# Optimization experiments

Hardware: AMD Instinct MI355X
Metric: run time of the kernel (lower is better)

The kernel has to match this reference:

```python
import jax, jax.numpy as jnp
import numpy as np

B, CIN, CMID, H, W = 2, 64, 128, 96, 96
KWIN = 7          # attention_window
DIL = 1           # attention_stride (dilation)
GROUPS = 16
EPS = 1e-5
SCALE = float(np.sqrt(CMID))  # torch: math.sqrt(intermediate_channels), multiplies logits (NATTEN semantics)


def group_norm(x, w, b):
    # x: [B,C,H,W], 16 groups, per-channel affine
    Bx, C, Hx, Wx = x.shape
    xg = x.reshape(Bx, GROUPS, C // GROUPS, Hx, Wx)
    mu = xg.mean(axis=(2, 3, 4), keepdims=True)
    var = xg.var(axis=(2, 3, 4), keepdims=True)
    xg = (xg - mu) * jax.lax.rsqrt(var + EPS)
    return xg.reshape(Bx, C, Hx, Wx) * w[None, :, None, None] + b[None, :, None, None]


def neighborhood_attention_2d(q, k, v, ksz, scale):
    # q,k,v: [B,H,W,C]; NATTEN-style neighborhood attention, dilation=1.
    Hh, Ww = q.shape[1], q.shape[2]
    half = ksz // 2
    # window start per query, clipped so every query sees exactly ksz keys per axis
    si = jnp.clip(jnp.arange(Hh) - half, 0, Hh - ksz)          # [H]
    sj = jnp.clip(jnp.arange(Ww) - half, 0, Ww - ksz)          # [W]
    idx_i = si[:, None] + jnp.arange(ksz)[None, :]             # [H,k]
    idx_j = sj[:, None] + jnp.arange(ksz)[None, :]             # [W,k]
    kw = k[:, idx_i][:, :, :, idx_j]                           # [B,H,k,W,k,C]
    vw = v[:, idx_i][:, :, :, idx_j]                           # [B,H,k,W,k,C]
    logits = jnp.einsum('bijc,biajkc->bijak', q, kw) * scale   # [B,H,W,k,k]
    Bq = logits.shape[0]
    attn = jax.nn.softmax(logits.reshape(Bq, Hh, Ww, ksz * ksz), axis=-1)
    attn = attn.reshape(Bq, Hh, Ww, ksz, ksz)
    return jnp.einsum('bijak,biajkc->bijc', attn, vw)          # [B,H,W,C]


def setup_inputs() -> dict:
    key = jax.random.key(0)
    ks = jax.random.split(key, 6)

    def wtz(k, shape, fan):
        return (jax.random.normal(k, shape, jnp.float32) / np.sqrt(fan)).astype(jnp.float32)

    return {
        'x': jax.random.normal(ks[0], (B, CIN, H, W), jnp.float32),
        'gn_w': jnp.ones((CIN,), jnp.float32),
        'gn_b': jnp.zeros((CIN,), jnp.float32),
        'conv_w': wtz(ks[1], (CMID, CIN, 3, 3), CIN * 9),
        'conv_b': jnp.zeros((CMID,), jnp.float32),
        'q_w': wtz(ks[2], (CMID, CMID), CMID),
        'q_b': jnp.zeros((CMID,), jnp.float32),
        'k_w': wtz(ks[3], (CMID, CMID), CMID),
        'k_b': jnp.zeros((CMID,), jnp.float32),
        'v_w': wtz(ks[4], (CMID, CMID), CMID),
        'v_b': jnp.zeros((CMID,), jnp.float32),
    }


def reference(x, gn_w, gn_b, conv_w, conv_b, q_w, q_b, k_w, k_b, v_w, v_b):
    xn = group_norm(x, gn_w, gn_b)
    # 3x3 conv, padding=1 + exact GELU (torch nn.GELU default)
    f = jax.lax.conv_general_dilated(
        xn, conv_w, window_strides=(1, 1), padding=((1, 1), (1, 1)),
        dimension_numbers=('NCHW', 'OIHW', 'NCHW')) + conv_b[None, :, None, None]
    f = jax.nn.gelu(f, approximate=False)
    # 1x1 QKV convs
    q = jnp.einsum('bchw,oc->bohw', f, q_w) + q_b[None, :, None, None]
    k = jnp.einsum('bchw,oc->bohw', f, k_w) + k_b[None, :, None, None]
    v = jnp.einsum('bchw,oc->bohw', f, v_w) + v_b[None, :, None, None]
    # to NHWC (singleton head dim squeezed)
    qh = q.transpose(0, 2, 3, 1)
    kh = k.transpose(0, 2, 3, 1)
    vh = v.transpose(0, 2, 3, 1)
    ksz = min(KWIN, f.shape[2], f.shape[3])
    ksz -= 1 if ksz % 2 == 0 else 0
    out = neighborhood_attention_2d(qh, kh, vh, ksz, SCALE)
    return out.transpose(0, 3, 1, 2)  # back to NCHW
```

## Files before the change

kernel.cpp:

```cpp
#include <hip/hip_runtime.h>
#include <math.h>

#define Hh 96
#define Ww 96
#define HW 9216
#define CIN 64
#define CMID 128
#define NAT_SCALE 11.313708498984761f

typedef __attribute__((ext_vector_type(4))) float f32x4;
typedef __attribute__((ext_vector_type(8))) short short8;

__device__ __forceinline__ unsigned short f2bf(float x) {
    union { float f; unsigned u; } v; v.f = x;
    unsigned r = v.u + 0x7FFF + ((v.u >> 16) & 1);
    return (unsigned short)(r >> 16);
}
__device__ __forceinline__ float bf2f(unsigned short h) {
    union { unsigned u; float f; } v; v.u = (unsigned)h << 16;
    return v.f;
}

__global__ __launch_bounds__(256) void prep_kernel(const float* __restrict__ x,
    float2* __restrict__ partials,
    const float* __restrict__ cw, const float* __restrict__ qw,
    const float* __restrict__ kw_, const float* __restrict__ vw,
    unsigned short* __restrict__ wch, unsigned short* __restrict__ wcl,
    unsigned short* __restrict__ wqh, unsigned short* __restrict__ wql)
{
    int bid = blockIdx.x, tid = threadIdx.x;
    if (bid < 512) {
        size_t base = (size_t)(bid >> 4) * 36864 + (size_t)(bid & 15) * 2304;
        float s = 0.f, s2 = 0.f;
        #pragma unroll
        for (int i = 0; i < 9; ++i) {
            float v = x[base + i * 256 + tid];
            s += v; s2 += v * v;
        }
        #pragma unroll
        for (int d = 1; d < 64; d <<= 1) {
            s  += __shfl_xor(s, d);
            s2 += __shfl_xor(s2, d);
        }
        __shared__ float as[4], as2[4];
        int wid = tid >> 6, lane = tid & 63;
        if (lane == 0) { as[wid] = s; as2[wid] = s2; }
        __syncthreads();
        if (tid == 0) {
            float2 r = { as[0]+as[1]+as[2]+as[3], as2[0]+as2[1]+as2[2]+as2[3] };
            partials[bid] = r;
        }
    } else {
        int t = (bid - 512) * 256 + tid;
        if (t < 73728) {
            int e = t & 7, l = (t >> 3) & 63, fr = (t >> 9) & 1;
            int ocg = (t >> 10) & 3, s2 = t >> 12;
            int s = s2 >> 1, ch = s2 & 1;
            int oc = ocg * 32 + fr * 16 + (l & 15);
            int c  = ch * 32 + (l >> 4) * 8 + e;
            float v = cw[oc * 576 + c * 9 + s];
            unsigned short hi = f2bf(v);
            wch[t] = hi; wcl[t] = f2bf(v - bf2f(hi));
        } else {
            int t2 = t - 73728;
            int e = t2 & 7, l = (t2 >> 3) & 63, fr = (t2 >> 9) & 1;
            int ocg = (t2 >> 10) & 3, kc2 = (t2 >> 12) & 3, m = t2 >> 14;
            int oc = ocg * 32 + fr * 16 + (l & 15);
            int c  = kc2 * 32 + (l >> 4) * 8 + e;
            const float* W = (m == 0) ? qw : (m == 1) ? kw_ : vw;
            float v = W[oc * 128 + c];
            unsigned short hi = f2bf(v);
            wqh[t2] = hi; wql[t2] = f2bf(v - bf2f(hi));
        }
    }
}

#define MFMA3(ACC, AH, AL, BH, BL) \
    ACC = __builtin_amdgcn_mfma_f32_16x16x32_bf16(AL, BH, ACC, 0, 0, 0); \
    ACC = __builtin_amdgcn_mfma_f32_16x16x32_bf16(AH, BL, ACC, 0, 0, 0); \
    ACC = __builtin_amdgcn_mfma_f32_16x16x32_bf16(AH, BH, ACC, 0, 0, 0);

__global__ __launch_bounds__(256) void convqkv_kernel(
    const float* __restrict__ x, const float2* __restrict__ partials,
    const float* __restrict__ gw, const float* __restrict__ gb,
    const unsigned short* __restrict__ wch, const unsigned short* __restrict__ wcl,
    const float* __restrict__ cb,
    const unsigned short* __restrict__ wqh, const unsigned short* __restrict__ wql,
    const float* __restrict__ qbias, const float* __restrict__ kbias,
    const float* __restrict__ vbias,
    float* __restrict__ qo, float* __restrict__ ko, float* __restrict__ vo)
{
    __shared__ __align__(16) short ph_s[3840];
    __shared__ __align__(16) short pl_s[3840];
    __shared__ __align__(16) short fh_s[4096];
    __shared__ __align__(16) short fl_s[4096];
    __shared__ float sgld[32];
    int bid = blockIdx.x;
    int swz = (bid & 7) * 72 + (bid >> 3);
    int b = swz / 288, rem = swz - b * 288;
    int ty = rem / 12, tx = rem - ty * 12;
    int y0 = ty * 4, x0 = tx * 8;
    int tid = threadIdx.x;

    float raw[15];
    #pragma unroll
    for (int it = 0; it < 15; ++it) {
        int idx = it * 256 + tid;
        int c = idx / 60, p = idx - c * 60;
        int row = p / 10, col = p - row * 10;
        int gy = y0 - 1 + row, gx = x0 - 1 + col;
        float v = 0.f;
        if ((unsigned)gy < 96u && (unsigned)gx < 96u)
            v = x[((size_t)(b * CIN + c)) * HW + gy * Ww + gx];
        raw[it] = v;
    }

    {
        float2 pv = partials[b * 256 + tid];
        float s = pv.x, s2 = pv.y;
        #pragma unroll
        for (int d = 1; d < 16; d <<= 1) {
            s  += __shfl_xor(s, d);
            s2 += __shfl_xor(s2, d);
        }
        if ((tid & 15) == 0) {
            const float invN = 1.f / 36864.f;
            float mean = s * invN;
            float var  = s2 * invN - mean * mean;
            sgld[(tid >> 4) * 2]     = mean;
            sgld[(tid >> 4) * 2 + 1] = rsqrtf(var + 1e-5f);
        }
    }
    __syncthreads();

    #pragma unroll
    for (int it = 0; it < 15; ++it) {
        int idx = it * 256 + tid;
        int c = idx / 60, p = idx - c * 60;
        int row = p / 10, col = p - row * 10;
        int gy = y0 - 1 + row, gx = x0 - 1 + col;
        bool ok = ((unsigned)gy < 96u && (unsigned)gx < 96u);
        float val = ok ? ((raw[it] - sgld[(c >> 2) * 2]) * sgld[(c >> 2) * 2 + 1]
                          * gw[c] + gb[c]) : 0.f;
        unsigned short hi = f2bf(val);
        unsigned short lo = f2bf(val - bf2f(hi));
        int di = ((row * 10 + col) << 6) + ((((c >> 3) ^ (col & 7)) << 3) | (c & 7));
        ph_s[di] = (short)hi;
        pl_s[di] = (short)lo;
    }
    __syncthreads();

    int ocg = tid >> 6, l = tid & 63;
    int l15 = l & 15, l4 = l >> 4;
    int oc0 = ocg * 32;
    int p0 = l15, p1 = 16 + l15;
    int r0 = p0 >> 3, xc = p0 & 7;

    f32x4 c00 = {0.f,0.f,0.f,0.f}, c01 = {0.f,0.f,0.f,0.f};
    f32x4 c10 = {0.f,0.f,0.f,0.f}, c11 = {0.f,0.f,0.f,0.f};

    #pragma unroll 3
    for (int s = 0; s < 9; ++s) {
        int dy = s / 3, dx = s - dy * 3;
        int colA = xc + dx, cswz = (colA & 7) << 3;
        #pragma unroll
        for (int ch = 0; ch < 2; ++ch) {
            int gr = (ch * 4 + l4) << 3;
            int ai0 = (((r0 + dy) * 10 + colA) << 6) + (gr ^ cswz);
            int ai1 = (((r0 + 2 + dy) * 10 + colA) << 6) + (gr ^ cswz);
            short8 a0h = *(const short8*)&ph_s[ai0];
            short8 a0l = *(const short8*)&pl_s[ai0];
            short8 a1h = *(const short8*)&ph_s[ai1];
            short8 a1l = *(const short8*)&pl_s[ai1];
            int s2 = s * 2 + ch;
            int wb = ((s2 * 4 + ocg) * 2) * 512 + l * 8;
            short8 b0h = *(const short8*)(wch + wb);
            short8 b0l = *(const short8*)(wcl + wb);
            short8 b1h = *(const short8*)(wch + wb + 512);
            short8 b1l = *(const short8*)(wcl + wb + 512);
            MFMA3(c00, a0h, a0l, b0h, b0l)
            MFMA3(c01, a0h, a0l, b1h, b1l)
            MFMA3(c10, a1h, a1l, b0h, b0l)
            MFMA3(c11, a1h, a1l, b1h, b1l)
        }
    }

    float bias0 = cb[oc0 + l15], bias1 = cb[oc0 + 16 + l15];
    #pragma unroll
    for (int mf = 0; mf < 2; ++mf) {
        #pragma unroll
        for (int nf = 0; nf < 2; ++nf) {
            f32x4 a = (mf == 0) ? (nf == 0 ? c00 : c01) : (nf == 0 ? c10 : c11);
            float bs = nf == 0 ? bias0 : bias1;
            int oc = oc0 + nf * 16 + l15;
            #pragma unroll
            for (int rr = 0; rr < 4; ++rr) {
                int p = mf * 16 + l4 * 4 + rr;
                float v = a[rr] + bs;
                float g = 0.5f * v * (1.f + erff(v * 0.70710678118654752f));
                unsigned short hi = f2bf(g);
                unsigned short lo = f2bf(g - bf2f(hi));
                int di = p * 128 + ((((oc >> 3) ^ (p & 7)) << 3) | (oc & 7));
                fh_s[di] = (short)hi;
                fl_s[di] = (short)lo;
            }
        }
    }
    __syncthreads();

    int sw0 = (p0 & 7) << 3, sw1 = (p1 & 7) << 3;
    #pragma unroll 1
    for (int m = 0; m < 3; ++m) {
        const float* Bi = (m == 0) ? qbias : (m == 1) ? kbias : vbias;
        float* Om = (m == 0) ? qo : (m == 1) ? ko : vo;
        f32x4 d00 = {0.f,0.f,0.f,0.f}, d01 = {0.f,0.f,0.f,0.f};
        f32x4 d10 = {0.f,0.f,0.f,0.f}, d11 = {0.f,0.f,0.f,0.f};
        #pragma unroll
        for (int kc2 = 0; kc2 < 4; ++kc2) {
            int gr2 = (kc2 * 4 + l4) << 3;
            int i0 = p0 * 128 + (gr2 ^ sw0);
            int i1 = p1 * 128 + (gr2 ^ sw1);
            short8 ah0 = *(const short8*)&fh_s[i0];
            short8 al0 = *(const short8*)&fl_s[i0];
            short8 ah1 = *(const short8*)&fh_s[i1];
            short8 al1 = *(const short8*)&fl_s[i1];
            int wb = (((m * 4 + kc2) * 4 + ocg) * 2) * 512 + l * 8;
            short8 b0h = *(const short8*)(wqh + wb);
            short8 b0l = *(const short8*)(wql + wb);
            short8 b1h = *(const short8*)(wqh + wb + 512);
            short8 b1l = *(const short8*)(wql + wb + 512);
            MFMA3(d00, ah0, al0, b0h, b0l)
            MFMA3(d01, ah0, al0, b1h, b1l)
            MFMA3(d10, ah1, al1, b0h, b0l)
            MFMA3(d11, ah1, al1, b1h, b1l)
        }
        float bm0 = Bi[oc0 + l15], bm1 = Bi[oc0 + 16 + l15];
        #pragma unroll
        for (int mf = 0; mf < 2; ++mf) {
            #pragma unroll
            for (int nf = 0; nf < 2; ++nf) {
                f32x4 a = (mf == 0) ? (nf == 0 ? d00 : d01) : (nf == 0 ? d10 : d11);
                float bs = nf == 0 ? bm0 : bm1;
                int oc = oc0 + nf * 16 + l15;
                #pragma unroll
                for (int rr = 0; rr < 4; ++rr) {
                    int p = mf * 16 + l4 * 4 + rr;
                    int yy = y0 + (p >> 3), xx = x0 + (p & 7);
                    Om[((size_t)(b * HW + yy * Ww + xx)) * CMID + oc] = a[rr] + bs;
                }
            }
        }
    }
}

__global__ __launch_bounds__(256) void nat_kernel(const float* __restrict__ q,
    const float* __restrict__ k, const float* __restrict__ v,
    float* __restrict__ out)
{
    __shared__ __align__(16) float Kl[12800];
    int bid = blockIdx.x;
    int swz = (bid & 7) * 144 + (bid >> 3);
    int b = swz / 576, rem = swz - b * 576;
    int ti = rem / 24, tj = rem - ti * 24;
    int i0 = ti * 4, j0 = tj * 4;
    int ui = i0 - 3; ui = ui < 0 ? 0 : (ui > 86 ? 86 : ui);
    int uj = j0 - 3; uj = uj < 0 ? 0 : (uj > 86 ? 86 : uj);
    int tid = threadIdx.x;

    const float4* ksrc = (const float4*)k;
    float4* Kl4 = (float4*)Kl;
    #pragma unroll
    for (int it = 0; it < 13; ++it) {
        int idx = it * 256 + tid;
        if (idx < 3200) {
            int row = idx >> 5, c4 = idx & 31;
            int ur = row / 10, uc = row - ur * 10;
            size_t gp = ((size_t)(b * HW + (ui + ur) * Ww + (uj + uc))) * 32 + c4;
            Kl4[row * 32 + (c4 ^ (row & 7))] = ksrc[gp];
        }
    }
    __syncthreads();

    int wid = tid >> 6, lane = tid & 63;
    int gy = wid >> 1, gx = wid & 1;
    int iq0 = i0 + 2 * gy, jq0 = j0 + 2 * gx;

    int si0 = iq0 - 3; si0 = si0 < 0 ? 0 : (si0 > 89 ? 89 : si0);
    int si1 = iq0 - 2; si1 = si1 < 0 ? 0 : (si1 > 89 ? 89 : si1);
    int sj0 = jq0 - 3; sj0 = sj0 < 0 ? 0 : (sj0 > 89 ? 89 : sj0);
    int sj1 = jq0 - 2; sj1 = sj1 < 0 ? 0 : (sj1 > 89 ? 89 : sj1);
    int gsi = si0 > 88 ? 88 : si0;
    int gsj = sj0 > 88 ? 88 : sj0;
    int oi0 = si0 - gsi, oi1 = si1 - gsi, oj0 = sj0 - gsj, oj1 = sj1 - gsj;
    int goi = gsi - ui, goj = gsj - uj;

    int wr = lane >> 3, wc = lane & 7;
    int R = (goi + wr) * 10 + (goj + wc);
    int Rs = R * 32, Rx = R & 7;

    const float4* qp0 = (const float4*)(q + (size_t)(b * HW + iq0 * Ww + jq0) * CMID);
    float a0 = 0.f, a1 = 0.f, a2 = 0.f, a3 = 0.f;
    #pragma unroll 8
    for (int c = 0; c < 32; ++c) {
        float4 kv = Kl4[Rs + (c ^ Rx)];
        float4 q0 = qp0[c], q1 = qp0[c + 32], q2 = qp0[c + 3072], q3 = qp0[c + 3104];
        a0 = fmaf(q0.x, kv.x, a0); a0 = fmaf(q0.y, kv.y, a0);
        a0 = fmaf(q0.z, kv.z, a0); a0 = fmaf(q0.w, kv.w, a0);
        a1 = fmaf(q1.x, kv.x, a1); a1 = fmaf(q1.y, kv.y, a1);
        a1 = fmaf(q1.z, kv.z, a1); a1 = fmaf(q1.w, kv.w, a1);
        a2 = fmaf(q2.x, kv.x, a2); a2 = fmaf(q2.y, kv.y, a2);
        a2 = fmaf(q2.z, kv.z, a2); a2 = fmaf(q2.w, kv.w, a2);
        a3 = fmaf(q3.x, kv.x, a3); a3 = fmaf(q3.y, kv.y, a3);
        a3 = fmaf(q3.z, kv.z, a3); a3 = fmaf(q3.w, kv.w, a3);
    }

    float l0 = ((unsigned)(wr - oi0) <= 6u && (unsigned)(wc - oj0) <= 6u) ? a0 * NAT_SCALE : -INFINITY;
    float l1 = ((unsigned)(wr - oi0) <= 6u && (unsigned)(wc - oj1) <= 6u) ? a1 * NAT_SCALE : -INFINITY;
    float l2 = ((unsigned)(wr - oi1) <= 6u && (unsigned)(wc - oj0) <= 6u) ? a2 * NAT_SCALE : -INFINITY;
    float l3 = ((unsigned)(wr - oi1) <= 6u && (unsigned)(wc - oj1) <= 6u) ? a3 * NAT_SCALE : -INFINITY;
    float m0 = l0, m1 = l1, m2 = l2, m3 = l3;
    #pragma unroll
    for (int d = 1; d < 64; d <<= 1) {
        m0 = fmaxf(m0, __shfl_xor(m0, d)); m1 = fmaxf(m1, __shfl_xor(m1, d));
        m2 = fmaxf(m2, __shfl_xor(m2, d)); m3 = fmaxf(m3, __shfl_xor(m3, d));
    }
    float e0 = __expf(l0 - m0), e1 = __expf(l1 - m1);
    float e2 = __expf(l2 - m2), e3 = __expf(l3 - m3);
    float s0 = e0, s1 = e1, s2 = e2, s3 = e3;
    #pragma unroll
    for (int d = 1; d < 64; d <<= 1) {
        s0 += __shfl_xor(s0, d); s1 += __shfl_xor(s1, d);
        s2 += __shfl_xor(s2, d); s3 += __shfl_xor(s3, d);
    }
    float w0 = e0 / s0, w1 = e1 / s1, w2 = e2 / s2, w3 = e3 / s3;

    int base2 = b * HW + gsi * Ww + gsj;
    const float2* vbase = (const float2*)(v + (size_t)base2 * CMID);
    float2 o0 = {0.f, 0.f}, o1 = {0.f, 0.f}, o2 = {0.f, 0.f}, o3 = {0.f, 0.f};
    #pragma unroll
    for (int w = 0; w < 64; ++w) {
        int off = ((w >> 3) * Ww + (w & 7)) * 64;
        float2 vv = vbase[off + lane];
        float b0 = __shfl(w0, w), b1 = __shfl(w1, w);
        float b2 = __shfl(w2, w), b3 = __shfl(w3, w);
        o0.x = fmaf(b0, vv.x, o0.x); o0.y = fmaf(b0, vv.y, o0.y);
        o1.x = fmaf(b1, vv.x, o1.x); o1.y = fmaf(b1, vv.y, o1.y);
        o2.x = fmaf(b2, vv.x, o2.x); o2.y = fmaf(b2, vv.y, o2.y);
        o3.x = fmaf(b3, vv.x, o3.x); o3.y = fmaf(b3, vv.y, o3.y);
    }

    size_t ob = ((size_t)(b * CMID + 2 * lane)) * HW + iq0 * Ww + jq0;
    float2 r0 = {o0.x, o1.x}, r1 = {o0.y, o1.y};
    float2 r2 = {o2.x, o3.x}, r3 = {o2.y, o3.y};
    *(float2*)(out + ob)           = r0;
    *(float2*)(out + ob + HW)      = r1;
    *(float2*)(out + ob + Ww)      = r2;
    *(float2*)(out + ob + HW + Ww) = r3;
}

extern "C" void kernel_launch(void* const* d_in, const int* in_sizes, int n_in,
                              void* d_out, int out_size, void* d_ws, size_t ws_size,
                              hipStream_t stream) {
    const float* x      = (const float*)d_in[0];
    const float* gn_w   = (const float*)d_in[1];
    const float* gn_b   = (const float*)d_in[2];
    const float* conv_w = (const float*)d_in[3];
    const float* conv_b = (const float*)d_in[4];
    const float* q_w    = (const float*)d_in[5];
    const float* q_b    = (const float*)d_in[6];
    const float* k_w    = (const float*)d_in[7];
    const float* k_b    = (const float*)d_in[8];
    const float* v_w    = (const float*)d_in[9];
    const float* v_b    = (const float*)d_in[10];

    float* ws    = (float*)d_ws;
    float2* partials = (float2*)ws;
    float* qb_   = ws + 1024;
    float* kb_   = qb_ + (size_t)2 * CMID * HW;
    float* vb_   = kb_ + (size_t)2 * CMID * HW;
    unsigned short* wch = (unsigned short*)(vb_ + (size_t)2 * CMID * HW);
    unsigned short* wcl = wch + 73728;
    unsigned short* wqh = wcl + 73728;
    unsigned short* wql = wqh + 49152;

    prep_kernel<<<992, 256, 0, stream>>>(x, partials, conv_w, q_w, k_w, v_w,
                                         wch, wcl, wqh, wql);
    convqkv_kernel<<<576, 256, 0, stream>>>(x, partials, gn_w, gn_b,
                                            wch, wcl, conv_b,
                                            wqh, wql, q_b, k_b, v_b,
                                            qb_, kb_, vb_);
    nat_kernel<<<1152, 256, 0, stream>>>(qb_, kb_, vb_, (float*)d_out);
}
```

Before: 74.97 us.

## Stage conv/QKV weights through double-buffered LDS with 512-thread blocks

Raises convqkv_kernel from 256 to 512 threads, with 8 waves split across position groups and output-channel groups, so each wave owns one 16-position fragment instead of two. Weight tiles for the 3x3 conv and the QKV projections are no longer read straight from global memory by every wave. They are staged into a double-buffered LDS area: the next tile is prefetched into registers while the current one feeds the MFMAs. Each step now needs a __syncthreads, which adds 30 barriers, and LDS use grows by 32 KB per block, which may limit how many blocks fit on a CU.

```diff
diff --git a/kernel.cpp b/kernel.cpp
--- a/kernel.cpp
+++ b/kernel.cpp
@@ -80,7 +80,7 @@
     ACC = __builtin_amdgcn_mfma_f32_16x16x32_bf16(AH, BL, ACC, 0, 0, 0); \
     ACC = __builtin_amdgcn_mfma_f32_16x16x32_bf16(AH, BH, ACC, 0, 0, 0);
 
-__global__ __launch_bounds__(256) void convqkv_kernel(
+__global__ __launch_bounds__(512) void convqkv_kernel(
     const float* __restrict__ x, const float2* __restrict__ partials,
     const float* __restrict__ gw, const float* __restrict__ gb,
     const unsigned short* __restrict__ wch, const unsigned short* __restrict__ wcl,
@@ -94,6 +94,7 @@
     __shared__ __align__(16) short pl_s[3840];
     __shared__ __align__(16) short fh_s[4096];
     __shared__ __align__(16) short fl_s[4096];
+    __shared__ __align__(16) short wstage[2][2][4096];
     __shared__ float sgld[32];
     int bid = blockIdx.x;
     int swz = (bid & 7) * 72 + (bid >> 3);
@@ -102,20 +103,25 @@
     int y0 = ty * 4, x0 = tx * 8;
     int tid = threadIdx.x;
 
-    float raw[15];
-    #pragma unroll
-    for (int it = 0; it < 15; ++it) {
-        int idx = it * 256 + tid;
-        int c = idx / 60, p = idx - c * 60;
-        int row = p / 10, col = p - row * 10;
-        int gy = y0 - 1 + row, gx = x0 - 1 + col;
+    float raw[8];
+    #pragma unroll
+    for (int it = 0; it < 8; ++it) {
+        int idx = it * 512 + tid;
         float v = 0.f;
-        if ((unsigned)gy < 96u && (unsigned)gx < 96u)
-            v = x[((size_t)(b * CIN + c)) * HW + gy * Ww + gx];
+        if (idx < 3840) {
+            int c = idx / 60, p = idx - c * 60;
+            int row = p / 10, col = p - row * 10;
+            int gy = y0 - 1 + row, gx = x0 - 1 + col;
+            if ((unsigned)gy < 96u && (unsigned)gx < 96u)
+                v = x[((size_t)(b * CIN + c)) * HW + gy * Ww + gx];
+        }
         raw[it] = v;
     }
 
-    {
+    *(short8*)&wstage[0][0][tid * 8] = *(const short8*)(wch + tid * 8);
+    *(short8*)&wstage[0][1][tid * 8] = *(const short8*)(wcl + tid * 8);
+
+    if (tid < 256) {
         float2 pv = partials[b * 256 + tid];
         float s = pv.x, s2 = pv.y;
         #pragma unroll
@@ -134,68 +140,73 @@
     __syncthreads();
 
     #pragma unroll
-    for (int it = 0; it < 15; ++it) {
-        int idx = it * 256 + tid;
-        int c = idx / 60, p = idx - c * 60;
-        int row = p / 10, col = p - row * 10;
-        int gy = y0 - 1 + row, gx = x0 - 1 + col;
-        bool ok = ((unsigned)gy < 96u && (unsigned)gx < 96u);
-        float val = ok ? ((raw[it] - sgld[(c >> 2) * 2]) * sgld[(c >> 2) * 2 + 1]
-                          * gw[c] + gb[c]) : 0.f;
-        unsigned short hi = f2bf(val);
-        unsigned short lo = f2bf(val - bf2f(hi));
-        int di = ((row * 10 + col) << 6) + ((((c >> 3) ^ (col & 7)) << 3) | (c & 7));
-        ph_s[di] = (short)hi;
-        pl_s[di] = (short)lo;
+    for (int it = 0; it < 8; ++it) {
+        int idx = it * 512 + tid;
+        if (idx < 3840) {
+            int c = idx / 60, p = idx - c * 60;
+            int row = p / 10, col = p - row * 10;
+            int gy = y0 - 1 + row, gx = x0 - 1 + col;
+            bool ok = ((unsigned)gy < 96u && (unsigned)gx < 96u);
+            float val = ok ? ((raw[it] - sgld[(c >> 2) * 2]) * sgld[(c >> 2) * 2 + 1]
+                              * gw[c] + gb[c]) : 0.f;
+            unsigned short hi = f2bf(val);
+            unsigned short lo = f2bf(val - bf2f(hi));
+            int di = ((row * 10 + col) << 6) + ((((c >> 3) ^ (col & 7)) << 3) | (c & 7));
+            ph_s[di] = (short)hi;
+            pl_s[di] = (short)lo;
+        }
     }
     __syncthreads();
 
-    int ocg = tid >> 6, l = tid & 63;
+    int wid = tid >> 6, l = tid & 63;
+    int posg = wid >> 2, ocg = wid & 3;
     int l15 = l & 15, l4 = l >> 4;
     int oc0 = ocg * 32;
-    int p0 = l15, p1 = 16 + l15;
+    int p0 = posg * 16 + l15;
     int r0 = p0 >> 3, xc = p0 & 7;
-
-    f32x4 c00 = {0.f,0.f,0.f,0.f}, c01 = {0.f,0.f,0.f,0.f};
-    f32x4 c10 = {0.f,0.f,0.f,0.f}, c11 = {0.f,0.f,0.f,0.f};
-
-    #pragma unroll 3
-    for (int s = 0; s < 9; ++s) {
+    int bo0 = (ocg * 2) * 512 + l * 8;
+    int bo1 = (ocg * 2 + 1) * 512 + l * 8;
+    int cur = 0;
+
+    f32x4 c0 = {0.f,0.f,0.f,0.f}, c1 = {0.f,0.f,0.f,0.f};
+
+    for (int s2 = 0; s2 < 18; ++s2) {
+        int ns = s2 + 1;
+        const unsigned short* nsh = (ns < 18) ? (wch + ns * 4096) : wqh;
+        const unsigned short* nsl = (ns < 18) ? (wcl + ns * 4096) : wql;
+        short8 nh = *(const short8*)(nsh + tid * 8);
+        short8 nl = *(const short8*)(nsl + tid * 8);
+
+        int s = s2 >> 1, ch = s2 & 1;
         int dy = s / 3, dx = s - dy * 3;
         int colA = xc + dx, cswz = (colA & 7) << 3;
-        #pragma unroll
-        for (int ch = 0; ch < 2; ++ch) {
-            int gr = (ch * 4 + l4) << 3;
-            int ai0 = (((r0 + dy) * 10 + colA) << 6) + (gr ^ cswz);
-            int ai1 = (((r0 + 2 + dy) * 10 + colA) << 6) + (gr ^ cswz);
-            short8 a0h = *(const short8*)&ph_s[ai0];
-            short8 a0l = *(const short8*)&pl_s[ai0];
-            short8 a1h = *(const short8*)&ph_s[ai1];
-            short8 a1l = *(const short8*)&pl_s[ai1];
-            int s2 = s * 2 + ch;
-            int wb = ((s2 * 4 + ocg) * 2) * 512 + l * 8;
-            short8 b0h = *(const short8*)(wch + wb);
-            short8 b0l = *(const short8*)(wcl + wb);
-            short8 b1h = *(const short8*)(wch + wb + 512);
-            short8 b1l = *(const short8*)(wcl + wb + 512);
-            MFMA3(c00, a0h, a0l, b0h, b0l)
-            MFMA3(c01, a0h, a0l, b1h, b1l)
-            MFMA3(c10, a1h, a1l, b0h, b0l)
-            MFMA3(c11, a1h, a1l, b1h, b1l)
-        }
-    }
-
-    float bias0 = cb[oc0 + l15], bias1 = cb[oc0 + 16 + l15];
-    #pragma unroll
-    for (int mf = 0; mf < 2; ++mf) {
+        int gr = (ch * 4 + l4) << 3;
+        int ai = (((r0 + dy) * 10 + colA) << 6) + (gr ^ cswz);
+        short8 ah = *(const short8*)&ph_s[ai];
+        short8 al = *(const short8*)&pl_s[ai];
+        short8 b0h = *(const short8*)&wstage[cur][0][bo0];
+        short8 b0l = *(const short8*)&wstage[cur][1][bo0];
+        short8 b1h = *(const short8*)&wstage[cur][0][bo1];
+        short8 b1l = *(const short8*)&wstage[cur][1][bo1];
+        MFMA3(c0, ah, al, b0h, b0l)
+        MFMA3(c1, ah, al, b1h, b1l)
+
+        *(short8*)&wstage[cur ^ 1][0][tid * 8] = nh;
+        *(short8*)&wstage[cur ^ 1][1][tid * 8] = nl;
+        __syncthreads();
+        cur ^= 1;
+    }
+
+    {
+        float bias0 = cb[oc0 + l15], bias1 = cb[oc0 + 16 + l15];
         #pragma unroll
         for (int nf = 0; nf < 2; ++nf) {
-            f32x4 a = (mf == 0) ? (nf == 0 ? c00 : c01) : (nf == 0 ? c10 : c11);
+            f32x4 a = nf == 0 ? c0 : c1;
             float bs = nf == 0 ? bias0 : bias1;
             int oc = oc0 + nf * 16 + l15;
             #pragma unroll
             for (int rr = 0; rr < 4; ++rr) {
-                int p = mf * 16 + l4 * 4 + rr;
+                int p = posg * 16 + l4 * 4 + rr;
                 float v = a[rr] + bs;
                 float g = 0.5f * v * (1.f + erff(v * 0.70710678118654752f));
                 unsigned short hi = f2bf(g);
@@ -208,48 +219,54 @@
     }
     __syncthreads();
 
-    int sw0 = (p0 & 7) << 3, sw1 = (p1 & 7) << 3;
-    #pragma unroll 1
-    for (int m = 0; m < 3; ++m) {
-        const float* Bi = (m == 0) ? qbias : (m == 1) ? kbias : vbias;
-        float* Om = (m == 0) ? qo : (m == 1) ? ko : vo;
-        f32x4 d00 = {0.f,0.f,0.f,0.f}, d01 = {0.f,0.f,0.f,0.f};
-        f32x4 d10 = {0.f,0.f,0.f,0.f}, d11 = {0.f,0.f,0.f,0.f};
-        #pragma unroll
-        for (int kc2 = 0; kc2 < 4; ++kc2) {
-            int gr2 = (kc2 * 4 + l4) << 3;
-            int i0 = p0 * 128 + (gr2 ^ sw0);
-            int i1 = p1 * 128 + (gr2 ^ sw1);
-            short8 ah0 = *(const short8*)&fh_s[i0];
-            short8 al0 = *(const short8*)&fl_s[i0];
-            short8 ah1 = *(const short8*)&fh_s[i1];
-            short8 al1 = *(const short8*)&fl_s[i1];
-            int wb = (((m * 4 + kc2) * 4 + ocg) * 2) * 512 + l * 8;
-            short8 b0h = *(const short8*)(wqh + wb);
-            short8 b0l = *(const short8*)(wql + wb);
-            short8 b1h = *(const short8*)(wqh + wb + 512);
-            short8 b1l = *(const short8*)(wql + wb + 512);
-            MFMA3(d00, ah0, al0, b0h, b0l)
-            MFMA3(d01, ah0, al0, b1h, b1l)
-            MFMA3(d10, ah1, al1, b0h, b0l)
-            MFMA3(d11, ah1, al1, b1h, b1l)
-        }
-        float bm0 = Bi[oc0 + l15], bm1 = Bi[oc0 + 16 + l15];
-        #pragma unroll
-        for (int mf = 0; mf < 2; ++mf) {
+    int sw0 = (p0 & 7) << 3;
+    f32x4 d0 = {0.f,0.f,0.f,0.f}, d1 = {0.f,0.f,0.f,0.f};
+    for (int j = 0; j < 12; ++j) {
+        int m = j >> 2, kc2 = j & 3;
+        short8 nh, nl;
+        bool pf = (j + 1 < 12);
+        if (pf) {
+            nh = *(const short8*)(wqh + (j + 1) * 4096 + tid * 8);
+            nl = *(const short8*)(wql + (j + 1) * 4096 + tid * 8);
+        }
+
+        int gr2 = (kc2 * 4 + l4) << 3;
+        int i0 = p0 * 128 + (gr2 ^ sw0);
+        short8 ah = *(const short8*)&fh_s[i0];
+        short8 al = *(const short8*)&fl_s[i0];
+        short8 b0h = *(const short8*)&wstage[cur][0][bo0];
+        short8 b0l = *(const short8*)&wstage[cur][1][bo0];
+        short8 b1h = *(const short8*)&wstage[cur][0][bo1];
+        short8 b1l = *(const short8*)&wstage[cur][1][bo1];
+        MFMA3(d0, ah, al, b0h, b0l)
+        MFMA3(d1, ah, al, b1h, b1l)
+
+        if (kc2 == 3) {
+            const float* Bi = (m == 0) ? qbias : (m == 1) ? kbias : vbias;
+            float* Om = (m == 0) ? qo : (m == 1) ? ko : vo;
+            float bm0 = Bi[oc0 + l15], bm1 = Bi[oc0 + 16 + l15];
             #pragma unroll
             for (int nf = 0; nf < 2; ++nf) {
-                f32x4 a = (mf == 0) ? (nf == 0 ? d00 : d01) : (nf == 0 ? d10 : d11);
+                f32x4 a = nf == 0 ? d0 : d1;
                 float bs = nf == 0 ? bm0 : bm1;
                 int oc = oc0 + nf * 16 + l15;
                 #pragma unroll
                 for (int rr = 0; rr < 4; ++rr) {
-                    int p = mf * 16 + l4 * 4 + rr;
+                    int p = posg * 16 + l4 * 4 + rr;
                     int yy = y0 + (p >> 3), xx = x0 + (p & 7);
                     Om[((size_t)(b * HW + yy * Ww + xx)) * CMID + oc] = a[rr] + bs;
                 }
             }
-        }
+            f32x4 z = {0.f,0.f,0.f,0.f};
+            d0 = z; d1 = z;
+        }
+
+        if (pf) {
+            *(short8*)&wstage[cur ^ 1][0][tid * 8] = nh;
+            *(short8*)&wstage[cur ^ 1][1][tid * 8] = nl;
+        }
+        __syncthreads();
+        cur ^= 1;
     }
 }
 
@@ -385,7 +402,7 @@
 
     prep_kernel<<<992, 256, 0, stream>>>(x, partials, conv_w, q_w, k_w, v_w,
                                          wch, wcl, wqh, wql);
-    convqkv_kernel<<<576, 256, 0, stream>>>(x, partials, gn_w, gn_b,
+    convqkv_kernel<<<576, 512, 0, stream>>>(x, partials, gn_w, gn_b,
                                             wch, wcl, conv_b,
                                             wqh, wql, q_b, k_b, v_b,
                                             qb_, kb_, vb_);
```

Measured after the change: 87.54 us. 1.17x slower.

## Split conv/QKV reduction dimension across two wave groups with LDS reduction

Applied to the files above, without the earlier changes.

The conv+QKV kernel now launches 512 threads per block. The 8 waves split the K (input-channel) dimension in half, and partial accumulators are summed through a shared-memory reduction buffer. This doubles the waves available to hide MFMA and load latency on only 576 blocks. In exchange it adds about 17KB of LDS, extra barriers per QKV matrix, and idle waves during the epilogue, which may reduce occupancy.

```diff
diff --git a/kernel.cpp b/kernel.cpp
--- a/kernel.cpp
+++ b/kernel.cpp
@@ -80,7 +80,7 @@
     ACC = __builtin_amdgcn_mfma_f32_16x16x32_bf16(AH, BL, ACC, 0, 0, 0); \
     ACC = __builtin_amdgcn_mfma_f32_16x16x32_bf16(AH, BH, ACC, 0, 0, 0);
 
-__global__ __launch_bounds__(256) void convqkv_kernel(
+__global__ __launch_bounds__(512) void convqkv_kernel(
     const float* __restrict__ x, const float2* __restrict__ partials,
     const float* __restrict__ gw, const float* __restrict__ gb,
     const unsigned short* __restrict__ wch, const unsigned short* __restrict__ wcl,
@@ -94,6 +94,7 @@
     __shared__ __align__(16) short pl_s[3840];
     __shared__ __align__(16) short fh_s[4096];
     __shared__ __align__(16) short fl_s[4096];
+    __shared__ float red[4352];
     __shared__ float sgld[32];
     int bid = blockIdx.x;
     int swz = (bid & 7) * 72 + (bid >> 3);
@@ -102,20 +103,22 @@
     int y0 = ty * 4, x0 = tx * 8;
     int tid = threadIdx.x;
 
-    float raw[15];
-    #pragma unroll
-    for (int it = 0; it < 15; ++it) {
-        int idx = it * 256 + tid;
-        int c = idx / 60, p = idx - c * 60;
-        int row = p / 10, col = p - row * 10;
-        int gy = y0 - 1 + row, gx = x0 - 1 + col;
+    float raw[8];
+    #pragma unroll
+    for (int it = 0; it < 8; ++it) {
+        int idx = it * 512 + tid;
         float v = 0.f;
-        if ((unsigned)gy < 96u && (unsigned)gx < 96u)
-            v = x[((size_t)(b * CIN + c)) * HW + gy * Ww + gx];
+        if (idx < 3840) {
+            int c = idx / 60, p = idx - c * 60;
+            int row = p / 10, col = p - row * 10;
+            int gy = y0 - 1 + row, gx = x0 - 1 + col;
+            if ((unsigned)gy < 96u && (unsigned)gx < 96u)
+                v = x[((size_t)(b * CIN + c)) * HW + gy * Ww + gx];
+        }
         raw[it] = v;
     }
 
-    {
+    if (tid < 256) {
         float2 pv = partials[b * 256 + tid];
         float s = pv.x, s2 = pv.y;
         #pragma unroll
@@ -134,27 +137,31 @@
     __syncthreads();
 
     #pragma unroll
-    for (int it = 0; it < 15; ++it) {
-        int idx = it * 256 + tid;
-        int c = idx / 60, p = idx - c * 60;
-        int row = p / 10, col = p - row * 10;
-        int gy = y0 - 1 + row, gx = x0 - 1 + col;
-        bool ok = ((unsigned)gy < 96u && (unsigned)gx < 96u);
-        float val = ok ? ((raw[it] - sgld[(c >> 2) * 2]) * sgld[(c >> 2) * 2 + 1]
-                          * gw[c] + gb[c]) : 0.f;
-        unsigned short hi = f2bf(val);
-        unsigned short lo = f2bf(val - bf2f(hi));
-        int di = ((row * 10 + col) << 6) + ((((c >> 3) ^ (col & 7)) << 3) | (c & 7));
-        ph_s[di] = (short)hi;
-        pl_s[di] = (short)lo;
+    for (int it = 0; it < 8; ++it) {
+        int idx = it * 512 + tid;
+        if (idx < 3840) {
+            int c = idx / 60, p = idx - c * 60;
+            int row = p / 10, col = p - row * 10;
+            int gy = y0 - 1 + row, gx = x0 - 1 + col;
+            bool ok = ((unsigned)gy < 96u && (unsigned)gx < 96u);
+            float val = ok ? ((raw[it] - sgld[(c >> 2) * 2]) * sgld[(c >> 2) * 2 + 1]
+                              * gw[c] + gb[c]) : 0.f;
+            unsigned short hi = f2bf(val);
+            unsigned short lo = f2bf(val - bf2f(hi));
+            int di = ((row * 10 + col) << 6) + ((((c >> 3) ^ (col & 7)) << 3) | (c & 7));
+            ph_s[di] = (short)hi;
+            pl_s[di] = (short)lo;
+        }
     }
     __syncthreads();
 
-    int ocg = tid >> 6, l = tid & 63;
+    int wid = tid >> 6, l = tid & 63;
+    int ocg = wid & 3, k2 = wid >> 2;
     int l15 = l & 15, l4 = l >> 4;
     int oc0 = ocg * 32;
     int p0 = l15, p1 = 16 + l15;
     int r0 = p0 >> 3, xc = p0 & 7;
+    int rb = (ocg * 64 + l) * 17;
 
     f32x4 c00 = {0.f,0.f,0.f,0.f}, c01 = {0.f,0.f,0.f,0.f};
     f32x4 c10 = {0.f,0.f,0.f,0.f}, c11 = {0.f,0.f,0.f,0.f};
@@ -163,46 +170,62 @@
     for (int s = 0; s < 9; ++s) {
         int dy = s / 3, dx = s - dy * 3;
         int colA = xc + dx, cswz = (colA & 7) << 3;
-        #pragma unroll
-        for (int ch = 0; ch < 2; ++ch) {
-            int gr = (ch * 4 + l4) << 3;
-            int ai0 = (((r0 + dy) * 10 + colA) << 6) + (gr ^ cswz);
-            int ai1 = (((r0 + 2 + dy) * 10 + colA) << 6) + (gr ^ cswz);
-            short8 a0h = *(const short8*)&ph_s[ai0];
-            short8 a0l = *(const short8*)&pl_s[ai0];
-            short8 a1h = *(const short8*)&ph_s[ai1];
-            short8 a1l = *(const short8*)&pl_s[ai1];
-            int s2 = s * 2 + ch;
-            int wb = ((s2 * 4 + ocg) * 2) * 512 + l * 8;
-            short8 b0h = *(const short8*)(wch + wb);
-            short8 b0l = *(const short8*)(wcl + wb);
-            short8 b1h = *(const short8*)(wch + wb + 512);
-            short8 b1l = *(const short8*)(wcl + wb + 512);
-            MFMA3(c00, a0h, a0l, b0h, b0l)
-            MFMA3(c01, a0h, a0l, b1h, b1l)
-            MFMA3(c10, a1h, a1l, b0h, b0l)
-            MFMA3(c11, a1h, a1l, b1h, b1l)
-        }
-    }
-
-    float bias0 = cb[oc0 + l15], bias1 = cb[oc0 + 16 + l15];
-    #pragma unroll
-    for (int mf = 0; mf < 2; ++mf) {
-        #pragma unroll
-        for (int nf = 0; nf < 2; ++nf) {
-            f32x4 a = (mf == 0) ? (nf == 0 ? c00 : c01) : (nf == 0 ? c10 : c11);
-            float bs = nf == 0 ? bias0 : bias1;
-            int oc = oc0 + nf * 16 + l15;
+        int gr = (k2 * 4 + l4) << 3;
+        int ai0 = (((r0 + dy) * 10 + colA) << 6) + (gr ^ cswz);
+        int ai1 = (((r0 + 2 + dy) * 10 + colA) << 6) + (gr ^ cswz);
+        short8 a0h = *(const short8*)&ph_s[ai0];
+        short8 a0l = *(const short8*)&pl_s[ai0];
+        short8 a1h = *(const short8*)&ph_s[ai1];
+        short8 a1l = *(const short8*)&pl_s[ai1];
+        int s2 = s * 2 + k2;
+        int wb = ((s2 * 4 + ocg) * 2) * 512 + l * 8;
+        short8 b0h = *(const short8*)(wch + wb);
+        short8 b0l = *(const short8*)(wcl + wb);
+        short8 b1h = *(const short8*)(wch + wb + 512);
+        short8 b1l = *(const short8*)(wcl + wb + 512);
+        MFMA3(c00, a0h, a0l, b0h, b0l)
+        MFMA3(c01, a0h, a0l, b1h, b1l)
+        MFMA3(c10, a1h, a1l, b0h, b0l)
+        MFMA3(c11, a1h, a1l, b1h, b1l)
+    }
+
+    if (k2 == 1) {
+        #pragma unroll
+        for (int j = 0; j < 4; ++j) {
+            red[rb + j]      = c00[j];
+            red[rb + 4 + j]  = c01[j];
+            red[rb + 8 + j]  = c10[j];
+            red[rb + 12 + j] = c11[j];
+        }
+    }
+    __syncthreads();
+    if (k2 == 0) {
+        #pragma unroll
+        for (int j = 0; j < 4; ++j) {
+            c00[j] += red[rb + j];
+            c01[j] += red[rb + 4 + j];
+            c10[j] += red[rb + 8 + j];
+            c11[j] += red[rb + 12 + j];
+        }
+        float bias0 = cb[oc0 + l15], bias1 = cb[oc0 + 16 + l15];
+        #pragma unroll
+        for (int mf = 0; mf < 2; ++mf) {
             #pragma unroll
-            for (int rr = 0; rr < 4; ++rr) {
-                int p = mf * 16 + l4 * 4 + rr;
-                float v = a[rr] + bs;
-                float g = 0.5f * v * (1.f + erff(v * 0.70710678118654752f));
-                unsigned short hi = f2bf(g);
-                unsigned short lo = f2bf(g - bf2f(hi));
-                int di = p * 128 + ((((oc >> 3) ^ (p & 7)) << 3) | (oc & 7));
-                fh_s[di] = (short)hi;
-                fl_s[di] = (short)lo;
+            for (int nf = 0; nf < 2; ++nf) {
+                f32x4 a = (mf == 0) ? (nf == 0 ? c00 : c01) : (nf == 0 ? c10 : c11);
+                float bs = nf == 0 ? bias0 : bias1;
+                int oc = oc0 + nf * 16 + l15;
+                #pragma unroll
+                for (int rr = 0; rr < 4; ++rr) {
+                    int p = mf * 16 + l4 * 4 + rr;
+                    float v = a[rr] + bs;
+                    float g = 0.5f * v * (1.f + erff(v * 0.70710678118654752f));
+                    unsigned short hi = f2bf(g);
+                    unsigned short lo = f2bf(g - bf2f(hi));
+                    int di = p * 128 + ((((oc >> 3) ^ (p & 7)) << 3) | (oc & 7));
+                    fh_s[di] = (short)hi;
+                    fl_s[di] = (short)lo;
+                }
             }
         }
     }
@@ -211,12 +234,11 @@
     int sw0 = (p0 & 7) << 3, sw1 = (p1 & 7) << 3;
     #pragma unroll 1
     for (int m = 0; m < 3; ++m) {
-        const float* Bi = (m == 0) ? qbias : (m == 1) ? kbias : vbias;
-        float* Om = (m == 0) ? qo : (m == 1) ? ko : vo;
         f32x4 d00 = {0.f,0.f,0.f,0.f}, d01 = {0.f,0.f,0.f,0.f};
         f32x4 d10 = {0.f,0.f,0.f,0.f}, d11 = {0.f,0.f,0.f,0.f};
         #pragma unroll
-        for (int kc2 = 0; kc2 < 4; ++kc2) {
+        for (int kk = 0; kk < 2; ++kk) {
+            int kc2 = k2 * 2 + kk;
             int gr2 = (kc2 * 4 + l4) << 3;
             int i0 = p0 * 128 + (gr2 ^ sw0);
             int i1 = p1 * 128 + (gr2 ^ sw1);
@@ -234,22 +256,44 @@
             MFMA3(d10, ah1, al1, b0h, b0l)
             MFMA3(d11, ah1, al1, b1h, b1l)
         }
-        float bm0 = Bi[oc0 + l15], bm1 = Bi[oc0 + 16 + l15];
-        #pragma unroll
-        for (int mf = 0; mf < 2; ++mf) {
+        if (k2 == 1) {
             #pragma unroll
-            for (int nf = 0; nf < 2; ++nf) {
-                f32x4 a = (mf == 0) ? (nf == 0 ? d00 : d01) : (nf == 0 ? d10 : d11);
-                float bs = nf == 0 ? bm0 : bm1;
-                int oc = oc0 + nf * 16 + l15;
+            for (int j = 0; j < 4; ++j) {
+                red[rb + j]      = d00[j];
+                red[rb + 4 + j]  = d01[j];
+                red[rb + 8 + j]  = d10[j];
+                red[rb + 12 + j] = d11[j];
+            }
+        }
+        __syncthreads();
+        if (k2 == 0) {
+            #pragma unroll
+            for (int j = 0; j < 4; ++j) {
+                d00[j] += red[rb + j];
+                d01[j] += red[rb + 4 + j];
+                d10[j] += red[rb + 8 + j];
+                d11[j] += red[rb + 12 + j];
+            }
+            const float* Bi = (m == 0) ? qbias : (m == 1) ? kbias : vbias;
+            float* Om = (m == 0) ? qo : (m == 1) ? ko : vo;
+            float bm0 = Bi[oc0 + l15], bm1 = Bi[oc0 + 16 + l15];
+            #pragma unroll
+            for (int mf = 0; mf < 2; ++mf) {
                 #pragma unroll
-                for (int rr = 0; rr < 4; ++rr) {
-                    int p = mf * 16 + l4 * 4 + rr;
-                    int yy = y0 + (p >> 3), xx = x0 + (p & 7);
-                    Om[((size_t)(b * HW + yy * Ww + xx)) * CMID + oc] = a[rr] + bs;
+                for (int nf = 0; nf < 2; ++nf) {
+                    f32x4 a = (mf == 0) ? (nf == 0 ? d00 : d01) : (nf == 0 ? d10 : d11);
+                    float bs = nf == 0 ? bm0 : bm1;
+                    int oc = oc0 + nf * 16 + l15;
+                    #pragma unroll
+                    for (int rr = 0; rr < 4; ++rr) {
+                        int p = mf * 16 + l4 * 4 + rr;
+                        int yy = y0 + (p >> 3), xx = x0 + (p & 7);
+                        Om[((size_t)(b * HW + yy * Ww + xx)) * CMID + oc] = a[rr] + bs;
+                    }
                 }
             }
         }
+        __syncthreads();
     }
 }
 
@@ -385,7 +429,7 @@
 
     prep_kernel<<<992, 256, 0, stream>>>(x, partials, conv_w, q_w, k_w, v_w,
                                          wch, wcl, wqh, wql);
-    convqkv_kernel<<<576, 256, 0, stream>>>(x, partials, gn_w, gn_b,
+    convqkv_kernel<<<576, 512, 0, stream>>>(x, partials, gn_w, gn_b,
                                             wch, wcl, conv_b,
                                             wqh, wql, q_b, k_b, v_b,
                                             qb_, kb_, vb_);
```

After: 80.14 us. 6.9% more time.
